# Performance work log

Measured on AMD Instinct MI355X. Metric: run time of the kernel, lower is better.

The kernel has to match this reference:

```python
import jax, jax.numpy as jnp
import numpy as np

N_HEADS = 16

def setup_inputs() -> dict:
    key = jax.random.key(0)
    k1, k2, k3 = jax.random.split(key, 3)
    B, T, C = 2, 2048, 1024
    x = jax.random.normal(k1, (B, T, C), dtype=jnp.float32)
    W_qkv = jax.random.normal(k2, (3 * C, C), dtype=jnp.float32) * 0.02
    b_qkv = jnp.zeros((3 * C,), dtype=jnp.float32)
    W_proj = jax.random.normal(k3, (C, C), dtype=jnp.float32) * 0.02
    b_proj = jnp.zeros((C,), dtype=jnp.float32)
    return {"x": x, "W_qkv": W_qkv, "b_qkv": b_qkv, "W_proj": W_proj, "b_proj": b_proj}

def reference(x, W_qkv, b_qkv, W_proj, b_proj):
    B, T, C = x.shape
    H = N_HEADS
    hd = C // H
    # fused QKV projection: (B,T,3C)
    qkv = x @ W_qkv.T + b_qkv
    # mirror torch: reshape to (B,T,H,3*hd) then chunk along last dim
    qkv = qkv.reshape(B, T, H, 3 * hd)
    q, k, v = jnp.split(qkv, 3, axis=-1)  # each (B,T,H,hd)
    q = q / jnp.sqrt(jnp.asarray(hd, dtype=q.dtype))
    # scaled dot-product attention, non-causal, full matrix (faithful to source)
    att = jnp.einsum('bihd,bjhd->bhij', q, k)  # (B,H,T,T)
    att = jax.nn.softmax(att, axis=-1)
    out = jnp.einsum('bhij,bjhd->bihd', att, v)  # (B,T,H,hd)
    out = out.reshape(B, T, C)
    return out @ W_proj.T + b_proj
```

## Files before the change

### kernel.cpp

```cpp
#include <hip/hip_runtime.h>


typedef __bf16 bf16x4 __attribute__((ext_vector_type(4)));
typedef __bf16 bf16x8 __attribute__((ext_vector_type(8)));
typedef float  f32x4  __attribute__((ext_vector_type(4)));

#define AS1(p) ((const __attribute__((address_space(1))) void*)(p))
#define AS3(p) ((__attribute__((address_space(3))) void*)(p))

__global__ __launch_bounds__(256)
void cvt_all(const float* __restrict__ a, const float* __restrict__ b,
             const float* __restrict__ c, __bf16* __restrict__ oa,
             __bf16* __restrict__ ob, __bf16* __restrict__ oc,
             int na, int nb, int nc)
{
    const int total = (na + nb + nc) >> 2;
    const int stride = gridDim.x * blockDim.x;
    for (int i4 = blockIdx.x * blockDim.x + threadIdx.x; i4 < total; i4 += stride) {
        int i = i4 << 2;
        const float* src; __bf16* dst;
        if (i < na)               { src = a + i;             dst = oa + i; }
        else if (i < na + nb)     { src = b + (i - na);      dst = ob + (i - na); }
        else                      { src = c + (i - na - nb); dst = oc + (i - na - nb); }
        const float4 v = *(const float4*)src;
        bf16x4 o = { (__bf16)v.x, (__bf16)v.y, (__bf16)v.z, (__bf16)v.w };
        *(bf16x4*)dst = o;
    }
}

template<int MODE>
__global__ __launch_bounds__(256)
void gemm_bt(const __bf16* __restrict__ A, const __bf16* __restrict__ W,
             const float* __restrict__ bias, int M, int N, int K,
             __bf16* __restrict__ O0, __bf16* __restrict__ O1,
             __bf16* __restrict__ O2, float* __restrict__ Of)
{
    __shared__ __bf16 sA[128 * 64];
    __shared__ __bf16 sB[128 * 64];
    const int tid  = threadIdx.x;
    const int w    = tid >> 6, lane = tid & 63;
    const int g    = lane >> 4, r16 = lane & 15;
    const int lin  = blockIdx.y * gridDim.x + blockIdx.x;
    const int per  = (gridDim.x * gridDim.y) >> 3;
    const int nlin = (lin & 7) * per + (lin >> 3);
    const int tM   = (nlin / gridDim.x) * 128, tN = (nlin % gridDim.x) * 128;
    const int wr   = w >> 1, wc = w & 1;
    const int crow = lane >> 3;
    const int ccol = (lane & 7) * 8;

    f32x4 acc[4][4] = {};

    for (int k0 = 0; k0 < K; k0 += 64) {
#pragma unroll
        for (int c = w; c < 16; c += 4) {
            const __bf16* ga = A + (size_t)(tM + c * 8 + crow) * K + k0 + ccol;
            __builtin_amdgcn_global_load_lds(AS1(ga), AS3(&sA[c * 8 * 64]), 16, 0, 0);
            const __bf16* gb = W + (size_t)(tN + c * 8 + crow) * K + k0 + ccol;
            __builtin_amdgcn_global_load_lds(AS1(gb), AS3(&sB[c * 8 * 64]), 16, 0, 0);
        }
        __syncthreads();
#pragma unroll
        for (int kk = 0; kk < 2; ++kk) {
            bf16x8 a[4], b[4];
#pragma unroll
            for (int mf = 0; mf < 4; ++mf)
                a[mf] = *(const bf16x8*)&sA[(wr * 64 + mf * 16 + r16) * 64 + kk * 32 + g * 8];
#pragma unroll
            for (int nf = 0; nf < 4; ++nf)
                b[nf] = *(const bf16x8*)&sB[(wc * 64 + nf * 16 + r16) * 64 + kk * 32 + g * 8];
#pragma unroll
            for (int mf = 0; mf < 4; ++mf)
#pragma unroll
                for (int nf = 0; nf < 4; ++nf)
                    acc[mf][nf] = __builtin_amdgcn_mfma_f32_16x16x32_bf16(
                        a[mf], b[nf], acc[mf][nf], 0, 0, 0);
        }
        __syncthreads();
    }

#pragma unroll
    for (int mf = 0; mf < 4; ++mf) {
#pragma unroll
        for (int nf = 0; nf < 4; ++nf) {
#pragma unroll
            for (int reg = 0; reg < 4; ++reg) {
                const int row = tM + wr * 64 + mf * 16 + g * 4 + reg;
                const int col = tN + wc * 64 + nf * 16 + r16;
                float v = acc[mf][nf][reg] + bias[col];
                if (MODE == 0) {
                    const int h = col / 192, j = col % 192;
                    const int b = row >> 11, t = row & 2047;
                    const size_t bh = (size_t)(b * 16 + h);
                    if (j < 64)
                        O0[(bh * 2048 + t) * 64 + j] = (__bf16)(v * 0.18033688011112042f);
                    else if (j < 128)
                        O1[(bh * 2048 + t) * 64 + (j - 64)] = (__bf16)v;
                    else
                        O2[(bh * 64 + (j - 128)) * 2048 + t] = (__bf16)v;
                } else {
                    Of[(size_t)row * N + col] = v;
                }
            }
        }
    }
}

__global__ __launch_bounds__(256, 4)
void attn(const __bf16* __restrict__ Q, const __bf16* __restrict__ K,
          const __bf16* __restrict__ V, __bf16* __restrict__ O)
{
    __shared__ __bf16 sK[2][64 * 64];
    __shared__ __bf16 sV[2][64 * 64];
    __shared__ __bf16 sP[64 * 64];

    const int tid = threadIdx.x;
    const int w   = tid >> 6, lane = tid & 63;
    const int g   = lane >> 4, r16 = lane & 15;
    const int m   = blockIdx.x + (blockIdx.y << 5) + (blockIdx.z << 9);
    const int bh  = (m & 7) + ((m >> 8) << 3);
    const int qb  = (m >> 3) & 31;
    const int q0  = qb * 64 + w * 16;
    const __bf16* Qp = Q + (size_t)bh * 2048 * 64;
    const __bf16* Kp = K + (size_t)bh * 2048 * 64;
    const __bf16* Vp = V + (size_t)bh * 64 * 2048;

    const int srow = lane >> 3;
    const int scol = 8 * ((lane & 7) ^ srow);
    const int swz  = (r16 & 7) << 4;
    char* const Pb = (char*)sP + (w * 16 + r16) * 128;

    bf16x8 qa[2];
#pragma unroll
    for (int kk = 0; kk < 2; ++kk)
        qa[kk] = *(const bf16x8*)(Qp + (size_t)(q0 + r16) * 64 + kk * 32 + g * 8);

    f32x4 o[4] = {};
    float mrun = -1e30f, lrun = 0.f;

#pragma unroll
    for (int r = 0; r < 2; ++r) {
        const int ldsb = r * 4096 + w * 1024;
        const int row  = r * 32 + w * 8 + srow;
        __builtin_amdgcn_global_load_lds(AS1(Kp + (size_t)row * 64 + scol),
                                         AS3((char*)&sK[0][0] + ldsb), 16, 0, 0);
        __builtin_amdgcn_global_load_lds(AS1(Vp + (size_t)row * 2048 + scol),
                                         AS3((char*)&sV[0][0] + ldsb), 16, 0, 0);
    }
    __syncthreads();

    for (int t = 0; t < 32; ++t) {
        const int cur = t & 1;
        if (t < 31) {
            const int kvn = (t + 1) * 64;
#pragma unroll
            for (int r = 0; r < 2; ++r) {
                const int ldsb = r * 4096 + w * 1024;
                const int row  = r * 32 + w * 8 + srow;
                __builtin_amdgcn_global_load_lds(AS1(Kp + (size_t)(kvn + row) * 64 + scol),
                                                 AS3((char*)&sK[cur ^ 1][0] + ldsb), 16, 0, 0);
                __builtin_amdgcn_global_load_lds(AS1(Vp + (size_t)row * 2048 + kvn + scol),
                                                 AS3((char*)&sV[cur ^ 1][0] + ldsb), 16, 0, 0);
            }
        }
        bf16x8 kb[4][2];
#pragma unroll
        for (int nf = 0; nf < 4; ++nf) {
            const int row = nf * 16 + r16;
#pragma unroll
            for (int kk = 0; kk < 2; ++kk)
                kb[nf][kk] = *(const bf16x8*)((const char*)&sK[cur][0] + row * 128
                                              + ((kk * 64 + g * 16) ^ swz));
        }
        f32x4 S[4];
        __builtin_amdgcn_s_setprio(1);
#pragma unroll
        for (int nf = 0; nf < 4; ++nf) {
            f32x4 s = {};
            s = __builtin_amdgcn_mfma_f32_16x16x32_bf16(kb[nf][0], qa[0], s, 0, 0, 0);
            s = __builtin_amdgcn_mfma_f32_16x16x32_bf16(kb[nf][1], qa[1], s, 0, 0, 0);
            S[nf] = s;
        }
        __builtin_amdgcn_s_setprio(0);
        float rm = fmaxf(fmaxf(S[0][0], S[0][1]), fmaxf(S[0][2], S[0][3]));
#pragma unroll
        for (int nf = 1; nf < 4; ++nf)
            rm = fmaxf(rm, fmaxf(fmaxf(S[nf][0], S[nf][1]), fmaxf(S[nf][2], S[nf][3])));
        rm = fmaxf(rm, __shfl_xor(rm, 16));
        rm = fmaxf(rm, __shfl_xor(rm, 32));
        if (!__all(rm <= mrun + 8.f)) {
            const float mn = fmaxf(mrun, rm);
            const float al = exp2f(mrun - mn);
#pragma unroll
            for (int df = 0; df < 4; ++df)
#pragma unroll
                for (int reg = 0; reg < 4; ++reg) o[df][reg] *= al;
            lrun *= al;
            mrun = mn;
        }
        float ps = 0.f;
#pragma unroll
        for (int nf = 0; nf < 4; ++nf)
#pragma unroll
            for (int reg = 0; reg < 4; ++reg) {
                const float p = exp2f(S[nf][reg] - mrun);
                S[nf][reg] = p;
                ps += p;
            }
        lrun += ps;
        asm volatile("s_waitcnt lgkmcnt(0)" ::: "memory");
        __builtin_amdgcn_sched_barrier(0);
#pragma unroll
        for (int nf = 0; nf < 4; ++nf) {
            bf16x4 pk = { (__bf16)S[nf][0], (__bf16)S[nf][1],
                          (__bf16)S[nf][2], (__bf16)S[nf][3] };
            *(bf16x4*)(Pb + ((nf * 32 + g * 8) ^ swz)) = pk;
        }
        asm volatile("s_waitcnt lgkmcnt(0)" ::: "memory");
        __builtin_amdgcn_sched_barrier(0);
        bf16x8 pb[2];
#pragma unroll
        for (int kk = 0; kk < 2; ++kk)
            pb[kk] = *(const bf16x8*)(Pb + ((kk * 64 + g * 16) ^ swz));
        __builtin_amdgcn_s_setprio(1);
#pragma unroll
        for (int kk = 0; kk < 2; ++kk)
#pragma unroll
            for (int df = 0; df < 4; ++df) {
                const int row = df * 16 + r16;
                bf16x8 vb = *(const bf16x8*)((const char*)&sV[cur][0] + row * 128
                                             + ((kk * 64 + g * 16) ^ swz));
                o[df] = __builtin_amdgcn_mfma_f32_16x16x32_bf16(vb, pb[kk], o[df], 0, 0, 0);
            }
        __builtin_amdgcn_s_setprio(0);
        __syncthreads();
    }

    lrun += __shfl_xor(lrun, 16);
    lrun += __shfl_xor(lrun, 32);
    const float inv = 1.f / lrun;
    const size_t token = (size_t)(bh >> 4) * 2048 + q0 + r16;
#pragma unroll
    for (int df = 0; df < 4; ++df) {
        bf16x4 ov = { (__bf16)(o[df][0] * inv), (__bf16)(o[df][1] * inv),
                      (__bf16)(o[df][2] * inv), (__bf16)(o[df][3] * inv) };
        *(bf16x4*)(O + token * 1024 + (bh & 15) * 64 + df * 16 + g * 4) = ov;
    }
}

extern "C" void kernel_launch(void* const* d_in, const int* in_sizes, int n_in,
                              void* d_out, int out_size, void* d_ws, size_t ws_size,
                              hipStream_t stream)
{
    const float* x     = (const float*)d_in[0];
    const float* Wqkv  = (const float*)d_in[1];
    const float* bqkv  = (const float*)d_in[2];
    const float* Wproj = (const float*)d_in[3];
    const float* bproj = (const float*)d_in[4];
    float* out = (float*)d_out;

    const size_t NX   = (size_t)4096 * 1024;
    const size_t NWQ  = (size_t)3072 * 1024;
    const size_t NWP  = (size_t)1024 * 1024;

    __bf16* xb  = (__bf16*)d_ws;
    __bf16* Wqb = xb  + NX;
    __bf16* Wpb = Wqb + NWQ;
    __bf16* Qs  = Wpb + NWP;
    __bf16* Ks  = Qs  + NX;
    __bf16* Vt  = Ks  + NX;
    __bf16* Os  = Vt  + NX;

    cvt_all<<<dim3(2048), dim3(256), 0, stream>>>(x, Wqkv, Wproj, xb, Wqb, Wpb,
                                                  (int)NX, (int)NWQ, (int)NWP);
    gemm_bt<0><<<dim3(24, 32), dim3(256), 0, stream>>>(xb, Wqb, bqkv, 4096, 3072, 1024, Qs, Ks, Vt, nullptr);
    attn<<<dim3(32, 16, 2), dim3(256), 0, stream>>>(Qs, Ks, Vt, Os);
    gemm_bt<1><<<dim3(8, 32), dim3(256), 0, stream>>>(Os, Wpb, bproj, 4096, 1024, 1024, nullptr, nullptr, nullptr, out);
}
```

Measured before the change: 148.6 us.

## Keep softmax probabilities in registers by permuting K rows to match MFMA layout

Drops the shared-memory round trip for the P tile: it was written to LDS and read back as the B operand of the PV MFMA. K rows are now permuted when loaded into the S MFMA, so each lane's S accumulator outputs line up with the key ordering the PV MFMA operand expects, and P is packed straight from registers. The K swizzle and global-load column mapping are changed to match the new row order. This removes LDS writes and reads plus two lgkmcnt waits per iteration, and frees the sP allocation. The cost is more complex indexing and a risk of bank conflicts or a wrong K/V pairing if the permutation is off.

```diff
diff --git a/kernel.cpp b/kernel.cpp
--- a/kernel.cpp
+++ b/kernel.cpp
@@ -111,7 +111,6 @@
 {
     __shared__ __bf16 sK[2][64 * 64];
     __shared__ __bf16 sV[2][64 * 64];
-    __shared__ __bf16 sP[64 * 64];
 
     const int tid = threadIdx.x;
     const int w   = tid >> 6, lane = tid & 63;
@@ -124,10 +123,11 @@
     const __bf16* Kp = K + (size_t)bh * 2048 * 64;
     const __bf16* Vp = V + (size_t)bh * 64 * 2048;
 
-    const int srow = lane >> 3;
-    const int scol = 8 * ((lane & 7) ^ srow);
-    const int swz  = (r16 & 7) << 4;
-    char* const Pb = (char*)sP + (w * 16 + r16) * 128;
+    const int srow  = lane >> 3;
+    const int scolV = 8 * ((lane & 7) ^ srow);
+    const int scolK = 8 * ((lane & 7) ^ ((srow & 3) | ((w & 1) << 2)));
+    const int swzK  = ((r16 & 3) | (((r16 >> 2) & 1) << 2)) << 4;
+    const int swzV  = (r16 & 7) << 4;
 
     bf16x8 qa[2];
 #pragma unroll
@@ -141,9 +141,9 @@
     for (int r = 0; r < 2; ++r) {
         const int ldsb = r * 4096 + w * 1024;
         const int row  = r * 32 + w * 8 + srow;
-        __builtin_amdgcn_global_load_lds(AS1(Kp + (size_t)row * 64 + scol),
+        __builtin_amdgcn_global_load_lds(AS1(Kp + (size_t)row * 64 + scolK),
                                          AS3((char*)&sK[0][0] + ldsb), 16, 0, 0);
-        __builtin_amdgcn_global_load_lds(AS1(Vp + (size_t)row * 2048 + scol),
+        __builtin_amdgcn_global_load_lds(AS1(Vp + (size_t)row * 2048 + scolV),
                                          AS3((char*)&sV[0][0] + ldsb), 16, 0, 0);
     }
     __syncthreads();
@@ -156,20 +156,20 @@
             for (int r = 0; r < 2; ++r) {
                 const int ldsb = r * 4096 + w * 1024;
                 const int row  = r * 32 + w * 8 + srow;
-                __builtin_amdgcn_global_load_lds(AS1(Kp + (size_t)(kvn + row) * 64 + scol),
+                __builtin_amdgcn_global_load_lds(AS1(Kp + (size_t)(kvn + row) * 64 + scolK),
                                                  AS3((char*)&sK[cur ^ 1][0] + ldsb), 16, 0, 0);
-                __builtin_amdgcn_global_load_lds(AS1(Vp + (size_t)row * 2048 + kvn + scol),
+                __builtin_amdgcn_global_load_lds(AS1(Vp + (size_t)row * 2048 + kvn + scolV),
                                                  AS3((char*)&sV[cur ^ 1][0] + ldsb), 16, 0, 0);
             }
         }
         bf16x8 kb[4][2];
 #pragma unroll
         for (int nf = 0; nf < 4; ++nf) {
-            const int row = nf * 16 + r16;
+            const int row = ((nf >> 1) << 5) + ((r16 >> 2) << 3) + ((nf & 1) << 2) + (r16 & 3);
 #pragma unroll
             for (int kk = 0; kk < 2; ++kk)
                 kb[nf][kk] = *(const bf16x8*)((const char*)&sK[cur][0] + row * 128
-                                              + ((kk * 64 + g * 16) ^ swz));
+                                              + ((kk * 64 + g * 16) ^ swzK));
         }
         f32x4 S[4];
         __builtin_amdgcn_s_setprio(1);
@@ -207,20 +207,16 @@
                 ps += p;
             }
         lrun += ps;
-        asm volatile("s_waitcnt lgkmcnt(0)" ::: "memory");
-        __builtin_amdgcn_sched_barrier(0);
-#pragma unroll
-        for (int nf = 0; nf < 4; ++nf) {
-            bf16x4 pk = { (__bf16)S[nf][0], (__bf16)S[nf][1],
-                          (__bf16)S[nf][2], (__bf16)S[nf][3] };
-            *(bf16x4*)(Pb + ((nf * 32 + g * 8) ^ swz)) = pk;
-        }
-        asm volatile("s_waitcnt lgkmcnt(0)" ::: "memory");
-        __builtin_amdgcn_sched_barrier(0);
         bf16x8 pb[2];
 #pragma unroll
-        for (int kk = 0; kk < 2; ++kk)
-            pb[kk] = *(const bf16x8*)(Pb + ((kk * 64 + g * 16) ^ swz));
+        for (int kk = 0; kk < 2; ++kk) {
+            bf16x8 tpk;
+            tpk[0] = (__bf16)S[kk * 2][0];     tpk[1] = (__bf16)S[kk * 2][1];
+            tpk[2] = (__bf16)S[kk * 2][2];     tpk[3] = (__bf16)S[kk * 2][3];
+            tpk[4] = (__bf16)S[kk * 2 + 1][0]; tpk[5] = (__bf16)S[kk * 2 + 1][1];
+            tpk[6] = (__bf16)S[kk * 2 + 1][2]; tpk[7] = (__bf16)S[kk * 2 + 1][3];
+            pb[kk] = tpk;
+        }
         __builtin_amdgcn_s_setprio(1);
 #pragma unroll
         for (int kk = 0; kk < 2; ++kk)
@@ -228,7 +224,7 @@
             for (int df = 0; df < 4; ++df) {
                 const int row = df * 16 + r16;
                 bf16x8 vb = *(const bf16x8*)((const char*)&sV[cur][0] + row * 128
-                                             + ((kk * 64 + g * 16) ^ swz));
+                                             + ((kk * 64 + g * 16) ^ swzV));
                 o[df] = __builtin_amdgcn_mfma_f32_16x16x32_bf16(vb, pb[kk], o[df], 0, 0, 0);
             }
         __builtin_amdgcn_s_setprio(0);
```

New measurement: 144.0 us. 1.03x faster.
